# Kernel optimization log

Measured on AMD Instinct MI355X. Metric: run time of the kernel, lower is better.

Reference implementation:

```python
import math
import jax, jax.numpy as jnp
import numpy as np

N_HEADS = 8
N_POINTS = 4


def bilinear_sample(img, gx, gy):
    """torch F.grid_sample(bilinear, align_corners=True, padding='zeros').
    img: [N,C,H,W]; gx,gy: [N,P] normalized coords (gx -> width axis, gy -> height axis).
    Returns [N,C,P]."""
    N, C, H, W = img.shape
    ix = (gx + 1.0) * 0.5 * (W - 1)
    iy = (gy + 1.0) * 0.5 * (H - 1)
    x0 = jnp.floor(ix); y0 = jnp.floor(iy)
    x1 = x0 + 1.0;      y1 = y0 + 1.0

    def corner(yc, xc, w):
        m = (xc >= 0) & (xc <= W - 1) & (yc >= 0) & (yc <= H - 1)
        xi = jnp.clip(xc, 0, W - 1).astype(jnp.int32)
        yi = jnp.clip(yc, 0, H - 1).astype(jnp.int32)
        v = jax.vmap(lambda im, y, x: im[:, y, x])(img, yi, xi)  # [N,C,P]
        return v * (w * m)[:, None, :]

    return (corner(y0, x0, (x1 - ix) * (y1 - iy))
            + corner(y0, x1, (ix - x0) * (y1 - iy))
            + corner(y1, x0, (x1 - ix) * (iy - y0))
            + corner(y1, x1, (ix - x0) * (iy - y0)))


def forward(query, points, features, cam_M, cam_b, W_off, b_off,
            W_q, b_q, W_k, b_k, W_v, b_v, W_o, b_o):
    B, K, C = query.shape
    ncam = features.shape[0]
    H, W = features.shape[-2:]
    nh, npnt = N_HEADS, N_POINTS
    hd = C // nh
    HW = jnp.asarray([H, W], dtype=query.dtype)

    # camera model: pixel = sigmoid(points @ M^T + b) * [H, W]   -> [ncam,B,K,2]
    px = jax.nn.sigmoid(jnp.einsum('bkj,cij->cbki', points, cam_M)
                        + cam_b[:, None, None, :]) * HW

    # ---- step 1: sample raw features at projected points (per camera) ----
    # original normalizes coord0 by H and coord1 by W (coord0 is grid_sample's x/width axis)
    gx1 = 2.0 * px[..., 0] / H - 1.0          # [ncam,B,K]
    gy1 = 2.0 * px[..., 1] / W - 1.0
    camf = jax.vmap(bilinear_sample)(features, gx1, gy1)   # [ncam,B,C,K]
    camf = jnp.transpose(camf, (1, 3, 0, 2))               # [B,K,ncam,C]

    query_ = query[:, :, None, :] + camf                   # [B,K,ncam,C]
    offsets = (query_ @ W_off.T + b_off).reshape(B, K, ncam, nh, npnt, 2)

    # ---- 1x1 conv key/value projections ----
    kf = (jnp.einsum('cbdhw,ed->cbehw', features, W_k)
          + b_k[None, None, :, None, None]).reshape(ncam, B * nh, hd, H, W)
    vf = (jnp.einsum('cbdhw,ed->cbehw', features, W_v)
          + b_v[None, None, :, None, None]).reshape(ncam, B * nh, hd, H, W)

    # ---- sampling locations with offsets ----
    off = jnp.moveaxis(offsets, 2, 0) / HW                 # [ncam,B,K,nh,np,2]
    pc = px[:, :, :, None, None, :] + off                  # [ncam,B,K,nh,np,2]
    gx = 2.0 * (pc[..., 0] / H) - 1.0
    gy = 2.0 * (pc[..., 1] / W) - 1.0
    # [ncam,B,K,nh,np] -> [ncam, B*nh, K*np]
    gx = jnp.transpose(gx, (0, 1, 3, 2, 4)).reshape(ncam, B * nh, K * npnt)
    gy = jnp.transpose(gy, (0, 1, 3, 2, 4)).reshape(ncam, B * nh, K * npnt)

    keys = jax.vmap(bilinear_sample)(kf, gx, gy)           # [ncam,B*nh,hd,K*np]
    vals = jax.vmap(bilinear_sample)(vf, gx, gy)

    def rearr(t):  # -> [B, nh, K, ncam*np, hd]
        t = t.reshape(ncam, B, nh, hd, K, npnt)
        return jnp.transpose(t, (1, 2, 4, 0, 5, 3)).reshape(B, nh, K, ncam * npnt, hd)

    keys, vals = rearr(keys), rearr(vals)

    q = (query @ W_q.T + b_q).reshape(B, K, nh, hd).transpose(0, 2, 1, 3)  # [B,nh,K,hd]
    logits = jnp.einsum('bhkd,bhkld->bhkl', q, keys) / math.sqrt(hd)
    attn = jax.nn.softmax(logits, axis=-1)
    weighted = jnp.einsum('bhkl,bhkld->bhkd', attn, vals)  # [B,nh,K,hd]
    # faithful to original torch `.view(B, K, embed_dim)` on a [B,nh,K,hd] tensor
    weighted = weighted.reshape(B, K, C)
    return weighted @ W_o.T + b_o


def setup_inputs() -> dict:
    key = jax.random.key(0)
    ks = jax.random.split(key, 16)
    B, K, C = 8, 900, 256
    ncam, H, W = 6, 32, 88
    f = lambda i, shape, s=1.0: jax.random.normal(ks[i], shape, dtype=jnp.float32) * s
    return {
        'query': f(0, (B, K, C)),
        'points': f(1, (B, K, 3)),
        'features': f(2, (ncam, B, C, H, W)),
        'cam_M': f(3, (ncam, 2, 3), 0.5),
        'cam_b': f(4, (ncam, 2), 0.5),
        'W_off': f(5, (2 * N_HEADS * N_POINTS, C), 0.02),
        'b_off': f(6, (2 * N_HEADS * N_POINTS,), 1.0),
        'W_q': f(7, (C, C), 0.02), 'b_q': f(8, (C,), 0.02),
        'W_k': f(9, (C, C), 0.02), 'b_k': f(10, (C,), 0.02),
        'W_v': f(11, (C, C), 0.02), 'b_v': f(12, (C,), 0.02),
        'W_o': f(13, (C, C), 0.02), 'b_o': f(14, (C,), 0.02),
    }


def reference(query, points, features, cam_M, cam_b, W_off, b_off,
              W_q, b_q, W_k, b_k, W_v, b_v, W_o, b_o):
    return forward(query, points, features, cam_M, cam_b, W_off, b_off,
                   W_q, b_q, W_k, b_k, W_v, b_v, W_o, b_o)
```

## Files before the change

kernel.cpp:

```cpp
#include <hip/hip_runtime.h>

typedef __attribute__((ext_vector_type(4))) float f32x4;
typedef __attribute__((ext_vector_type(8))) short bf16x8;
typedef __attribute__((ext_vector_type(4))) unsigned int u32x4;

__device__ __forceinline__ unsigned short f2bf(float f) {
    union { float f; unsigned int u; } x; x.f = f;
    unsigned int u = x.u;
    return (unsigned short)((u + 0x7FFFu + ((u >> 16) & 1u)) >> 16);
}
__device__ __forceinline__ float bf2f(unsigned short b) {
    union { unsigned int u; float f; } x; x.u = ((unsigned int)b) << 16;
    return x.f;
}
__device__ __forceinline__ float u2f(unsigned int u) {
    union { unsigned int u; float f; } x; x.u = u; return x.f;
}


__global__ void prep_all(const float* __restrict__ Wk, const float* __restrict__ bk,
                         const float* __restrict__ Wv, const float* __restrict__ bv,
                         const float* __restrict__ Wq, const float* __restrict__ bq,
                         const float* __restrict__ Woff, const float* __restrict__ boff,
                         unsigned short* __restrict__ Wkv, float* __restrict__ bkv,
                         unsigned short* __restrict__ Woffp,
                         float* __restrict__ Wcat, float* __restrict__ bcat) {
    int i = blockIdx.x * 256 + threadIdx.x;
    if (i < 512 * 256) {
        int n = i >> 8, k = i & 255;
        float v = (n < 256) ? Wk[i] : Wv[i - 65536];
        Wkv[((size_t)(n >> 7) * 8 + (k >> 5)) * 4096 + (n & 127) * 32 + (k & 31)] = f2bf(v);
    }
    if (i < 512) bkv[i] = (i < 256) ? bk[i] : bv[i - 256];
    if (i < 64 * 256) {
        int n = i >> 8, k = i & 255;
        Woffp[(size_t)(k >> 5) * 4096 + n * 32 + (k & 31)] = f2bf(Woff[i]);
    }
    if (i < 320 * 256) Wcat[i] = (i < 65536) ? Wq[i] : Woff[i - 65536];
    if (i < 320) bcat[i] = (i < 256) ? bq[i] : boff[i - 256];
}

__global__ __launch_bounds__(256) void transpose_feat(const float* __restrict__ src,
                                                      unsigned short* __restrict__ dst) {
    __shared__ float tile[32][33];
    int img = blockIdx.z;
    int p0 = blockIdx.x * 32;
    int d0 = blockIdx.y * 32;
    int tx = threadIdx.x & 31, ty = threadIdx.x >> 5;
    const float* s = src + (size_t)img * 256 * 2816;
#pragma unroll
    for (int i = 0; i < 4; i++) tile[ty + 8 * i][tx] = s[(size_t)(d0 + ty + 8 * i) * 2816 + p0 + tx];
    __syncthreads();
    int m = img * 2816 + p0;
    unsigned short* o = dst + ((size_t)(m >> 7) * 8 + (d0 >> 5)) * 4096 + (m & 127) * 32;
#pragma unroll
    for (int i = 0; i < 4; i++) o[(ty + 8 * i) * 32 + tx] = f2bf(tile[tx][ty + 8 * i]);
}

__global__ __launch_bounds__(256) void gemm_kv2(
    const unsigned short* __restrict__ A,
    const unsigned short* __restrict__ Wkv,
    const unsigned short* __restrict__ Woffp,
    const float* __restrict__ bias,
    unsigned short* __restrict__ C,
    float* __restrict__ Foff) {
    __shared__ __align__(16) unsigned short Bl[16384];
    __shared__ __align__(16) unsigned short Ar[3][4096];

    const int tid = threadIdx.x, lane = tid & 63, w = tid >> 6;
    const int lrow = lane & 15, lk = lane >> 4;
    const int lsw = (lane >> 2) * 32 + (((lane & 3) ^ ((lane >> 3) & 3)) * 8);
    const int ckx = ((lrow >> 1) & 3);
    const int bid = blockIdx.x;
    const int wgid = (bid & 7) * 660 + (bid >> 3);
    const int chunk = wgid / 5, bn = wgid % 5;

    const unsigned short* A0 = A + (size_t)chunk * 32768;
    const unsigned short* BbK = (bn < 4)
        ? Wkv + (size_t)(bn >> 1) * 32768 + (bn & 1) * 2048
        : Woffp;
    const unsigned short* BbV = (bn < 4)
        ? Wkv + (size_t)((bn + 4) >> 1) * 32768 + ((bn + 4) & 1) * 2048
        : Woffp;
    const int wof = w * 1024;

#define STAGE_B(HALF)                                                                        \
    {                                                                                        \
        _Pragma("unroll")                                                                    \
        for (int i = 0; i < 4; ++i) {                                                        \
            __builtin_amdgcn_global_load_lds(                                                \
                (const __attribute__((address_space(1))) unsigned int*)(BbK + ((HALF) * 4 + w) * 4096 + i * 512 + lsw), \
                (__attribute__((address_space(3))) unsigned int*)&Bl[w * 4096 + i * 512], 16, 0, 0);                    \
        }                                                                                    \
        _Pragma("unroll")                                                                    \
        for (int i = 0; i < 4; ++i) {                                                        \
            __builtin_amdgcn_global_load_lds(                                                \
                (const __attribute__((address_space(1))) unsigned int*)(BbV + ((HALF) * 4 + w) * 4096 + i * 512 + lsw), \
                (__attribute__((address_space(3))) unsigned int*)&Bl[w * 4096 + 2048 + i * 512], 16, 0, 0);             \
        }                                                                                    \
    }

#define STAGE_STEP(S)                                                                        \
    {                                                                                        \
        __builtin_amdgcn_global_load_lds(                                                    \
            (const __attribute__((address_space(1))) unsigned int*)(A0 + (S) * 4096 + wof + lsw),        \
            (__attribute__((address_space(3))) unsigned int*)&Ar[(S) % 3][wof], 16, 0, 0);   \
        __builtin_amdgcn_global_load_lds(                                                    \
            (const __attribute__((address_space(1))) unsigned int*)(A0 + (S) * 4096 + wof + 512 + lsw),  \
            (__attribute__((address_space(3))) unsigned int*)&Ar[(S) % 3][wof + 512], 16, 0, 0);         \
    }

    STAGE_B(0)
    STAGE_STEP(0) STAGE_STEP(1)
    __syncthreads();

    f32x4 acc[2][8] = {};

#define COMP_STEP(S, NW)                                                                     \
    {                                                                                        \
        asm volatile("s_waitcnt vmcnt(%0)" :: "i"(NW) : "memory");                           \
        bf16x8 bfr[8], af[2];                                                                \
        _Pragma("unroll") for (int j = 0; j < 4; ++j)                                        \
            bfr[j] = *(const bf16x8*)&Bl[((S) & 3) * 4096 + (j * 16 + lrow) * 32 + (lk ^ ckx) * 8];          \
        _Pragma("unroll") for (int j = 0; j < 4; ++j)                                        \
            bfr[4 + j] = *(const bf16x8*)&Bl[((S) & 3) * 4096 + 2048 + (j * 16 + lrow) * 32 + (lk ^ ckx) * 8]; \
        _Pragma("unroll") for (int i = 0; i < 2; ++i)                                        \
            af[i] = *(const bf16x8*)&Ar[(S) % 3][wof + i * 512 + lrow * 32 + (lk ^ ckx) * 8];\
        if ((S) + 2 < 8) {                                                                   \
            asm volatile("s_waitcnt lgkmcnt(0)" ::: "memory");                               \
            STAGE_STEP((S) + 2)                                                              \
        }                                                                                    \
        _Pragma("unroll") for (int i = 0; i < 2; ++i)                                        \
            _Pragma("unroll") for (int j = 0; j < 8; ++j)                                    \
                acc[i][j] = __builtin_amdgcn_mfma_f32_16x16x32_bf16(af[i], bfr[j], acc[i][j], 0, 0, 0); \
    }

    COMP_STEP(0, 4) COMP_STEP(1, 2) COMP_STEP(2, 2) COMP_STEP(3, 2)
    __syncthreads();
    STAGE_B(1)
    __syncthreads();
    COMP_STEP(4, 4) COMP_STEP(5, 2) COMP_STEP(6, 2) COMP_STEP(7, 0)
#undef COMP_STEP
#undef STAGE_STEP
#undef STAGE_B

    if (bn < 4) {
        unsigned short* Cl = &Bl[0];
        __syncthreads();
#pragma unroll
        for (int j = 0; j < 8; ++j) {
            float bs = (j < 4) ? bias[bn * 64 + j * 16 + lrow]
                               : bias[(bn + 4) * 64 + (j - 4) * 16 + lrow];
#pragma unroll
            for (int i = 0; i < 2; ++i)
#pragma unroll
                for (int jj = 0; jj < 4; ++jj)
                    Cl[(w * 32 + i * 16 + lk * 4 + jj) * 128 + j * 16 + lrow] =
                        f2bf(acc[i][j][jj] + bs);
        }
        __syncthreads();
#pragma unroll
        for (int it = 0; it < 8; ++it) {
            int idx = it * 256 + tid;
            int px = idx >> 4, d = idx & 15;
            int s = (d < 4) ? d : (d < 8) ? d + 4 : (d < 12) ? d - 4 : d;
            *(f32x4*)(C + (size_t)(chunk * 128 + px) * 512 + bn * 128 + d * 8) =
                *(const f32x4*)&Cl[px * 128 + s * 8];
        }
    } else {
#pragma unroll
        for (int i = 0; i < 2; ++i)
#pragma unroll
            for (int j = 0; j < 4; ++j)
#pragma unroll
                for (int jj = 0; jj < 4; ++jj) {
                    int m = chunk * 128 + w * 32 + i * 16 + lk * 4 + jj;
                    Foff[(size_t)m * 64 + j * 16 + lrow] = acc[i][j][jj];
                }
    }
}

template <bool SPLIT, bool C_BF16>
__global__ __launch_bounds__(256) void gemm_bf16(
    const float* __restrict__ A, long long aBatch,
    const float* __restrict__ B, const float* __restrict__ bias,
    void* __restrict__ Cv, long long cBatch,
    int M, int N, int K, int lda) {
    __shared__ __align__(16) unsigned short Ah[64][40];
    __shared__ __align__(16) unsigned short Bh[64][40];
    __shared__ __align__(16) unsigned short Al[(SPLIT ? 64 : 1)][40];
    __shared__ __align__(16) unsigned short Bl[(SPLIT ? 64 : 1)][40];

    const int tid = threadIdx.x;
    const int m0 = blockIdx.x * 64, n0 = blockIdx.y * 64;
    const int batch = blockIdx.z;
    const float* Ab = A + (size_t)batch * aBatch;
    const int lane = tid & 63, wave = tid >> 6;
    const int wr = wave & 1, wc = wave >> 1;
    const int lrow = lane & 15, lk = lane >> 4;

    f32x4 acc[2][2] = {};

    for (int kt = 0; kt < K; kt += 32) {
        if (kt) __syncthreads();
        {
            int c4 = (tid & 7) * 4;
#pragma unroll
            for (int rep = 0; rep < 2; rep++) {
                int r = (tid >> 3) + rep * 32;
                int m = m0 + r; if (m >= M) m = M - 1;
                f32x4 v = *(const f32x4*)(Ab + (size_t)m * lda + kt + c4);
#pragma unroll
                for (int q = 0; q < 4; q++) {
                    unsigned short h = f2bf(v[q]);
                    Ah[r][c4 + q] = h;
                    if (SPLIT) Al[r][c4 + q] = f2bf(v[q] - bf2f(h));
                }
            }
        }
        {
            int c4 = (tid & 7) * 4;
#pragma unroll
            for (int rep = 0; rep < 2; rep++) {
                int r = (tid >> 3) + rep * 32;
                f32x4 v = *(const f32x4*)(B + (size_t)(n0 + r) * K + kt + c4);
#pragma unroll
                for (int q = 0; q < 4; q++) {
                    unsigned short h = f2bf(v[q]);
                    Bh[r][c4 + q] = h;
                    if (SPLIT) Bl[r][c4 + q] = f2bf(v[q] - bf2f(h));
                }
            }
        }
        __syncthreads();

        bf16x8 a_h[2], b_h[2], a_l[2], b_l[2];
#pragma unroll
        for (int i = 0; i < 2; i++) {
            a_h[i] = *(const bf16x8*)&Ah[wr * 32 + i * 16 + lrow][lk * 8];
            b_h[i] = *(const bf16x8*)&Bh[wc * 32 + i * 16 + lrow][lk * 8];
            if (SPLIT) {
                a_l[i] = *(const bf16x8*)&Al[wr * 32 + i * 16 + lrow][lk * 8];
                b_l[i] = *(const bf16x8*)&Bl[wc * 32 + i * 16 + lrow][lk * 8];
            }
        }
#pragma unroll
        for (int i = 0; i < 2; i++)
#pragma unroll
            for (int j = 0; j < 2; j++) {
                acc[i][j] = __builtin_amdgcn_mfma_f32_16x16x32_bf16(a_h[i], b_h[j], acc[i][j], 0, 0, 0);
                if (SPLIT) {
                    acc[i][j] = __builtin_amdgcn_mfma_f32_16x16x32_bf16(a_h[i], b_l[j], acc[i][j], 0, 0, 0);
                    acc[i][j] = __builtin_amdgcn_mfma_f32_16x16x32_bf16(a_l[i], b_h[j], acc[i][j], 0, 0, 0);
                }
            }
    }

#pragma unroll
    for (int i = 0; i < 2; i++)
#pragma unroll
        for (int j = 0; j < 2; j++) {
            int n = n0 + wc * 32 + j * 16 + lrow;
            float bs = bias[n];
#pragma unroll
            for (int jj = 0; jj < 4; jj++) {
                int m = m0 + wr * 32 + i * 16 + lk * 4 + jj;
                if (m < M) {
                    float val = acc[i][j][jj] + bs;
                    if (C_BF16)
                        ((unsigned short*)Cv)[(size_t)batch * cBatch + (size_t)m * N + n] = f2bf(val);
                    else
                        ((float*)Cv)[(size_t)batch * cBatch + (size_t)m * N + n] = val;
                }
            }
        }
}

__global__ __launch_bounds__(512) void attn_kernel(
    const float* __restrict__ qcat, const float* __restrict__ points,
    const float* __restrict__ camM, const float* __restrict__ camb,
    const float* __restrict__ Foff, const unsigned short* __restrict__ kv_t,
    float* __restrict__ S) {
    int bk = blockIdx.x;
    int b = bk / 900, k = bk % 900;
    int h = threadIdx.x >> 6;
    int lane = threadIdx.x & 63;

    __shared__ __align__(16) float        ldsW[8][24][4];
    __shared__ __align__(16) unsigned int ldsI[8][24][4];
    __shared__ float ldsL[8][24];

    if (lane < 24) {
        int cam = lane >> 2, p = lane & 3;
        float pt0 = points[(size_t)bk * 3 + 0];
        float pt1 = points[(size_t)bk * 3 + 1];
        float pt2 = points[(size_t)bk * 3 + 2];
        const float* M = camM + cam * 6;
        float s0 = M[0] * pt0 + M[1] * pt1 + M[2] * pt2 + camb[cam * 2 + 0];
        float s1 = M[3] * pt0 + M[4] * pt1 + M[5] * pt2 + camb[cam * 2 + 1];
        float px0 = (1.f / (1.f + expf(-s0))) * 32.f;
        float px1 = (1.f / (1.f + expf(-s1))) * 88.f;
        {
            float gxb = 2.f * px0 / 32.f - 1.f, gyb = 2.f * px1 / 88.f - 1.f;
            float ixb = (gxb + 1.f) * 0.5f * 87.f;
            float iyb = (gyb + 1.f) * 0.5f * 31.f;
            float xb0 = floorf(ixb), yb0 = floorf(iyb), xb1 = xb0 + 1.f, yb1 = yb0 + 1.f;
            float wxb1 = ixb - xb0, wxb0 = xb1 - ixb, wyb1 = iyb - yb0, wyb0 = yb1 - iyb;
            float mb00 = (xb0 >= 0.f && xb0 <= 87.f && yb0 >= 0.f && yb0 <= 31.f) ? 1.f : 0.f;
            float mb01 = (xb1 >= 0.f && xb1 <= 87.f && yb0 >= 0.f && yb0 <= 31.f) ? 1.f : 0.f;
            float mb10 = (xb0 >= 0.f && xb0 <= 87.f && yb1 >= 0.f && yb1 <= 31.f) ? 1.f : 0.f;
            float mb11 = (xb1 >= 0.f && xb1 <= 87.f && yb1 >= 0.f && yb1 <= 31.f) ? 1.f : 0.f;
            float wb00 = wxb0 * wyb0 * mb00, wb01 = wxb1 * wyb0 * mb01;
            float wb10 = wxb0 * wyb1 * mb10, wb11 = wxb1 * wyb1 * mb11;
            int xib0 = (int)fminf(fmaxf(xb0, 0.f), 87.f);
            int xib1 = (int)fminf(fmaxf(xb1, 0.f), 87.f);
            int yib0 = (int)fminf(fmaxf(yb0, 0.f), 31.f);
            int yib1 = (int)fminf(fmaxf(yb1, 0.f), 31.f);
            size_t base = (size_t)(cam * 8 + b) * 2816;
            const float* f00 = Foff + (base + yib0 * 88 + xib0) * 64;
            const float* f01 = Foff + (base + yib0 * 88 + xib1) * 64;
            const float* f10 = Foff + (base + yib1 * 88 + xib0) * 64;
            const float* f11 = Foff + (base + yib1 * 88 + xib1) * 64;
            int j0 = (h * 4 + p) * 2;
            float o0 = qcat[(size_t)bk * 320 + 256 + j0]
                     + wb00 * f00[j0] + wb01 * f01[j0] + wb10 * f10[j0] + wb11 * f11[j0];
            float o1 = qcat[(size_t)bk * 320 + 256 + j0 + 1]
                     + wb00 * f00[j0 + 1] + wb01 * f01[j0 + 1] + wb10 * f10[j0 + 1] + wb11 * f11[j0 + 1];
            float pc0 = px0 + o0 * (1.f / 32.f);
            float pc1 = px1 + o1 * (1.f / 88.f);
            float gx = 2.f * (pc0 * (1.f / 32.f)) - 1.f;
            float gy = 2.f * (pc1 * (1.f / 88.f)) - 1.f;
            float ix = (gx + 1.f) * 0.5f * 87.f;
            float iy = (gy + 1.f) * 0.5f * 31.f;
            float x0 = floorf(ix), y0 = floorf(iy), x1 = x0 + 1.f, y1 = y0 + 1.f;
            float wx1 = ix - x0, wx0 = x1 - ix, wy1 = iy - y0, wy0 = y1 - iy;
            float m00 = (x0 >= 0.f && x0 <= 87.f && y0 >= 0.f && y0 <= 31.f) ? 1.f : 0.f;
            float m01 = (x1 >= 0.f && x1 <= 87.f && y0 >= 0.f && y0 <= 31.f) ? 1.f : 0.f;
            float m10 = (x0 >= 0.f && x0 <= 87.f && y1 >= 0.f && y1 <= 31.f) ? 1.f : 0.f;
            float m11 = (x1 >= 0.f && x1 <= 87.f && y1 >= 0.f && y1 <= 31.f) ? 1.f : 0.f;
            int xi0 = (int)fminf(fmaxf(x0, 0.f), 87.f);
            int xi1 = (int)fminf(fmaxf(x1, 0.f), 87.f);
            int yi0 = (int)fminf(fmaxf(y0, 0.f), 31.f);
            int yi1 = (int)fminf(fmaxf(y1, 0.f), 31.f);
            unsigned int img = (unsigned int)(cam * 8 + b) * 2816u;
            ldsW[h][lane][0] = wx0 * wy0 * m00;
            ldsW[h][lane][1] = wx1 * wy0 * m01;
            ldsW[h][lane][2] = wx0 * wy1 * m10;
            ldsW[h][lane][3] = wx1 * wy1 * m11;
            ldsI[h][lane][0] = (img + yi0 * 88 + xi0) * 1024u;
            ldsI[h][lane][1] = (img + yi0 * 88 + xi1) * 1024u;
            ldsI[h][lane][2] = (img + yi1 * 88 + xi0) * 1024u;
            ldsI[h][lane][3] = (img + yi1 * 88 + xi1) * 1024u;
        }
    }
    __syncthreads();

    const int p8 = lane >> 3, dlane = lane & 7;
    const int chB = h * 128 + dlane * 16;
    const char* kvb = (const char*)kv_t;

    f32x4 qa = *(const f32x4*)(qcat + (size_t)bk * 320 + h * 32 + (dlane & 3) * 8);
    f32x4 qb = *(const f32x4*)(qcat + (size_t)bk * 320 + h * 32 + (dlane & 3) * 8 + 4);

    float vr[3][8];
    const float inv_sqrt = 0.17677669529663687f;
#pragma unroll
    for (int it = 0; it < 3; ++it) {
        int l = it * 8 + p8;
        f32x4 w = *(const f32x4*)ldsW[h][l];
        unsigned int i0 = ldsI[h][l][0], i1 = ldsI[h][l][1];
        unsigned int i2 = ldsI[h][l][2], i3 = ldsI[h][l][3];
        u32x4 u0 = *(const u32x4*)(kvb + i0 + chB);
        u32x4 u1 = *(const u32x4*)(kvb + i1 + chB);
        u32x4 u2 = *(const u32x4*)(kvb + i2 + chB);
        u32x4 u3 = *(const u32x4*)(kvb + i3 + chB);
#pragma unroll
        for (int q = 0; q < 4; ++q) {
            vr[it][2 * q] = w[0] * u2f(u0[q] << 16) + w[1] * u2f(u1[q] << 16)
                          + w[2] * u2f(u2[q] << 16) + w[3] * u2f(u3[q] << 16);
            vr[it][2 * q + 1] = w[0] * u2f(u0[q] & 0xFFFF0000u) + w[1] * u2f(u1[q] & 0xFFFF0000u)
                              + w[2] * u2f(u2[q] & 0xFFFF0000u) + w[3] * u2f(u3[q] & 0xFFFF0000u);
        }
        float t = qa[0] * vr[it][0] + qa[1] * vr[it][1] + qa[2] * vr[it][2] + qa[3] * vr[it][3]
                + qb[0] * vr[it][4] + qb[1] * vr[it][5] + qb[2] * vr[it][6] + qb[3] * vr[it][7];
        t += __shfl_xor(t, 1);
        t += __shfl_xor(t, 2);
        if (dlane == 0) ldsL[h][l] = t * inv_sqrt;
    }
    __syncthreads();

    float mx = -1e30f;
#pragma unroll
    for (int l = 0; l < 24; l++) mx = fmaxf(mx, ldsL[h][l]);
    float ssum = 0.f;
    float at3[3];
#pragma unroll
    for (int l = 0; l < 24; l++) {
        float e = __expf(ldsL[h][l] - mx);
        ssum += e;
        if ((l & 7) == p8) at3[l >> 3] = e;
    }
    float inv = 1.f / ssum;

    float o[8];
#pragma unroll
    for (int j = 0; j < 8; ++j)
        o[j] = at3[0] * vr[0][j] + at3[1] * vr[1][j] + at3[2] * vr[2][j];
#pragma unroll
    for (int j = 0; j < 8; ++j) {
        o[j] += __shfl_xor(o[j], 8);
        o[j] += __shfl_xor(o[j], 16);
        o[j] += __shfl_xor(o[j], 32);
    }
    if (p8 == 0 && dlane >= 4) {
        int d0 = (dlane - 4) * 8;
        f32x4 v0, v1;
        v0[0] = o[0] * inv; v0[1] = o[1] * inv; v0[2] = o[2] * inv; v0[3] = o[3] * inv;
        v1[0] = o[4] * inv; v1[1] = o[5] * inv; v1[2] = o[6] * inv; v1[3] = o[7] * inv;
        float* dst = &S[(size_t)b * 230400 + (size_t)h * 28800 + k * 32 + d0];
        *(f32x4*)dst = v0;
        *(f32x4*)(dst + 4) = v1;
    }
}

extern "C" void kernel_launch(void* const* d_in, const int* in_sizes, int n_in,
                              void* d_out, int out_size, void* d_ws, size_t ws_size,
                              hipStream_t stream) {
    const float* query    = (const float*)d_in[0];
    const float* points   = (const float*)d_in[1];
    const float* features = (const float*)d_in[2];
    const float* camM     = (const float*)d_in[3];
    const float* camb     = (const float*)d_in[4];
    const float* W_off    = (const float*)d_in[5];
    const float* b_off    = (const float*)d_in[6];
    const float* W_q      = (const float*)d_in[7];
    const float* b_q      = (const float*)d_in[8];
    const float* W_k      = (const float*)d_in[9];
    const float* b_k      = (const float*)d_in[10];
    const float* W_v      = (const float*)d_in[11];
    const float* b_v      = (const float*)d_in[12];
    const float* W_o      = (const float*)d_in[13];
    const float* b_o      = (const float*)d_in[14];

    char* ws = (char*)d_ws;
    unsigned short* feat_t = (unsigned short*)ws; ws += 69206016;
    unsigned short* kv_t   = (unsigned short*)ws; ws += 138412032;
    float* Foff   = (float*)ws; ws += 34603008;
    float* qcat   = (float*)ws; ws += 9216000;
    float* S      = (float*)ws; ws += 7372800;
    unsigned short* Wkv = (unsigned short*)ws; ws += 524288;
    float* bkv    = (float*)ws; ws += 2048;
    unsigned short* Woffp = (unsigned short*)ws; ws += 65536;
    float* Wcat   = (float*)ws; ws += 327680;
    float* bcat   = (float*)ws; ws += 1280;

    prep_all<<<512, 256, 0, stream>>>(W_k, b_k, W_v, b_v, W_q, b_q, W_off, b_off,
                                      Wkv, bkv, Woffp, Wcat, bcat);
    transpose_feat<<<dim3(88, 8, 48), 256, 0, stream>>>(features, feat_t);
    gemm_kv2<<<5280, 256, 0, stream>>>(feat_t, Wkv, Woffp, bkv, kv_t, Foff);
    gemm_bf16<true, false><<<dim3(113, 5, 1), 256, 0, stream>>>(
        query, 0, Wcat, bcat, qcat, 0, 7200, 320, 256, 256);
    attn_kernel<<<7200, 512, 0, stream>>>(qcat, points, camM, camb, Foff, kv_t, S);
    gemm_bf16<true, false><<<dim3(113, 4, 1), 256, 0, stream>>>(
        S, 0, W_o, b_o, d_out, 0, 7200, 256, 256, 256);
}
```

Measured before the change: 231.2 us.

## Halve B-tile LDS buffer in gemm_kv2 with quarter-staged weight loads

Shrinks the shared B weight buffer in the KV projection GEMM from 32 KB to 16 KB by staging the weights in four quarters instead of two halves. The epilogue is split into two passes so the smaller buffer can still hold the bf16 output. The lower LDS footprint is meant to let more workgroups stay resident per CU. In exchange it adds more block barriers and exposes weight-load latency, since each quarter is loaded between barriers without overlapping compute.

Result: slower. 236.3 us (+2.2%).

```diff
diff --git a/kernel.cpp b/kernel.cpp
--- a/kernel.cpp
+++ b/kernel.cpp
@@ -64,7 +64,7 @@
     const float* __restrict__ bias,
     unsigned short* __restrict__ C,
     float* __restrict__ Foff) {
-    __shared__ __align__(16) unsigned short Bl[16384];
+    __shared__ __align__(16) unsigned short Bl[8192];
     __shared__ __align__(16) unsigned short Ar[3][4096];
 
     const int tid = threadIdx.x, lane = tid & 63, w = tid >> 6;
@@ -84,19 +84,14 @@
         : Woffp;
     const int wof = w * 1024;
 
-#define STAGE_B(HALF)                                                                        \
+#define STAGE_BQ(Q)                                                                          \
     {                                                                                        \
+        const unsigned short* src = ((w & 1) ? BbV : BbK) + ((Q) * 2 + (w >> 1)) * 4096;     \
         _Pragma("unroll")                                                                    \
         for (int i = 0; i < 4; ++i) {                                                        \
             __builtin_amdgcn_global_load_lds(                                                \
-                (const __attribute__((address_space(1))) unsigned int*)(BbK + ((HALF) * 4 + w) * 4096 + i * 512 + lsw), \
-                (__attribute__((address_space(3))) unsigned int*)&Bl[w * 4096 + i * 512], 16, 0, 0);                    \
-        }                                                                                    \
-        _Pragma("unroll")                                                                    \
-        for (int i = 0; i < 4; ++i) {                                                        \
-            __builtin_amdgcn_global_load_lds(                                                \
-                (const __attribute__((address_space(1))) unsigned int*)(BbV + ((HALF) * 4 + w) * 4096 + i * 512 + lsw), \
-                (__attribute__((address_space(3))) unsigned int*)&Bl[w * 4096 + 2048 + i * 512], 16, 0, 0);             \
+                (const __attribute__((address_space(1))) unsigned int*)(src + i * 512 + lsw),\
+                (__attribute__((address_space(3))) unsigned int*)&Bl[(w >> 1) * 4096 + (w & 1) * 2048 + i * 512], 16, 0, 0); \
         }                                                                                    \
     }
 
@@ -110,20 +105,19 @@
             (__attribute__((address_space(3))) unsigned int*)&Ar[(S) % 3][wof + 512], 16, 0, 0);         \
     }
 
-    STAGE_B(0)
+    STAGE_BQ(0)
     STAGE_STEP(0) STAGE_STEP(1)
     __syncthreads();
 
     f32x4 acc[2][8] = {};
 
-#define COMP_STEP(S, NW)                                                                     \
+#define COMP_STEP(S)                                                                         \
     {                                                                                        \
-        asm volatile("s_waitcnt vmcnt(%0)" :: "i"(NW) : "memory");                           \
         bf16x8 bfr[8], af[2];                                                                \
         _Pragma("unroll") for (int j = 0; j < 4; ++j)                                        \
-            bfr[j] = *(const bf16x8*)&Bl[((S) & 3) * 4096 + (j * 16 + lrow) * 32 + (lk ^ ckx) * 8];          \
+            bfr[j] = *(const bf16x8*)&Bl[((S) & 1) * 4096 + (j * 16 + lrow) * 32 + (lk ^ ckx) * 8];          \
         _Pragma("unroll") for (int j = 0; j < 4; ++j)                                        \
-            bfr[4 + j] = *(const bf16x8*)&Bl[((S) & 3) * 4096 + 2048 + (j * 16 + lrow) * 32 + (lk ^ ckx) * 8]; \
+            bfr[4 + j] = *(const bf16x8*)&Bl[((S) & 1) * 4096 + 2048 + (j * 16 + lrow) * 32 + (lk ^ ckx) * 8]; \
         _Pragma("unroll") for (int i = 0; i < 2; ++i)                                        \
             af[i] = *(const bf16x8*)&Ar[(S) % 3][wof + i * 512 + lrow * 32 + (lk ^ ckx) * 8];\
         if ((S) + 2 < 8) {                                                                   \
@@ -135,37 +129,44 @@
                 acc[i][j] = __builtin_amdgcn_mfma_f32_16x16x32_bf16(af[i], bfr[j], acc[i][j], 0, 0, 0); \
     }
 
-    COMP_STEP(0, 4) COMP_STEP(1, 2) COMP_STEP(2, 2) COMP_STEP(3, 2)
-    __syncthreads();
-    STAGE_B(1)
-    __syncthreads();
-    COMP_STEP(4, 4) COMP_STEP(5, 2) COMP_STEP(6, 2) COMP_STEP(7, 0)
+    COMP_STEP(0) COMP_STEP(1)
+    __syncthreads(); STAGE_BQ(1) __syncthreads();
+    COMP_STEP(2) COMP_STEP(3)
+    __syncthreads(); STAGE_BQ(2) __syncthreads();
+    COMP_STEP(4) COMP_STEP(5)
+    __syncthreads(); STAGE_BQ(3) __syncthreads();
+    COMP_STEP(6) COMP_STEP(7)
 #undef COMP_STEP
 #undef STAGE_STEP
-#undef STAGE_B
+#undef STAGE_BQ
 
     if (bn < 4) {
         unsigned short* Cl = &Bl[0];
-        __syncthreads();
-#pragma unroll
-        for (int j = 0; j < 8; ++j) {
-            float bs = (j < 4) ? bias[bn * 64 + j * 16 + lrow]
-                               : bias[(bn + 4) * 64 + (j - 4) * 16 + lrow];
-#pragma unroll
-            for (int i = 0; i < 2; ++i)
-#pragma unroll
-                for (int jj = 0; jj < 4; ++jj)
-                    Cl[(w * 32 + i * 16 + lk * 4 + jj) * 128 + j * 16 + lrow] =
-                        f2bf(acc[i][j][jj] + bs);
-        }
-        __syncthreads();
-#pragma unroll
-        for (int it = 0; it < 8; ++it) {
-            int idx = it * 256 + tid;
-            int px = idx >> 4, d = idx & 15;
-            int s = (d < 4) ? d : (d < 8) ? d + 4 : (d < 12) ? d - 4 : d;
-            *(f32x4*)(C + (size_t)(chunk * 128 + px) * 512 + bn * 128 + d * 8) =
-                *(const f32x4*)&Cl[px * 128 + s * 8];
+#pragma unroll
+        for (int pteam = 0; pteam < 2; ++pteam) {
+            __syncthreads();
+            if ((w >> 1) == pteam) {
+#pragma unroll
+                for (int j = 0; j < 8; ++j) {
+                    float bs = (j < 4) ? bias[bn * 64 + j * 16 + lrow]
+                                       : bias[(bn + 4) * 64 + (j - 4) * 16 + lrow];
+#pragma unroll
+                    for (int i = 0; i < 2; ++i)
+#pragma unroll
+                        for (int jj = 0; jj < 4; ++jj)
+                            Cl[((w & 1) * 32 + i * 16 + lk * 4 + jj) * 128 + j * 16 + lrow] =
+                                f2bf(acc[i][j][jj] + bs);
+                }
+            }
+            __syncthreads();
+#pragma unroll
+            for (int it = 0; it < 4; ++it) {
+                int idx = it * 256 + tid;
+                int px = idx >> 4, d = idx & 15;
+                int s = (d < 4) ? d : (d < 8) ? d + 4 : (d < 12) ? d - 4 : d;
+                *(f32x4*)(C + (size_t)(chunk * 128 + pteam * 64 + px) * 512 + bn * 128 + d * 8) =
+                    *(const f32x4*)&Cl[px * 128 + s * 8];
+            }
         }
     } else {
 #pragma unroll
```
